# Kernel optimization log

Hardware: AMD Instinct MI355X
Metric: run time of the kernel (lower is better)

## Reference

```python
import jax, jax.numpy as jnp
import numpy as np

B, N, D = 16, 4096, 256
EPS = 1e-6


def setup_inputs() -> dict:
    key = jax.random.key(0)
    kq, kk, kv, kwq, kwk, kbq, kbk = jax.random.split(key, 7)
    s = 1.0 / np.sqrt(D)
    return {
        "Q": jax.random.normal(kq, (B, N, D), dtype=jnp.float32),
        "K": jax.random.normal(kk, (B, N, D), dtype=jnp.float32),
        "V": jax.random.normal(kv, (B, N, D), dtype=jnp.float32),
        "Wq": jax.random.normal(kwq, (D, D), dtype=jnp.float32) * s,
        "bq": jax.random.normal(kbq, (D,), dtype=jnp.float32) * 0.01,
        "Wk": jax.random.normal(kwk, (D, D), dtype=jnp.float32) * s,
        "bk": jax.random.normal(kbk, (D,), dtype=jnp.float32) * 0.01,
    }


def reference(Q, K, V, Wq, bq, Wk, bk):
    # phi feature maps: sigmoid(Linear(dim, dim)) as in Flow-Attention
    phi_q = jax.nn.sigmoid(jnp.einsum("bnd,de->bne", Q, Wq) + bq)  # [B,N,D]
    phi_k = jax.nn.sigmoid(jnp.einsum("bnd,de->bne", K, Wk) + bk)  # [B,N,D]
    # O: column-normalized phi_k (over sequence); I: row-normalized phi_q (over features)
    O = phi_k / (jnp.sum(phi_k, axis=1, keepdims=True) + EPS)  # [B,N,D]
    I = phi_q / (jnp.sum(phi_q, axis=2, keepdims=True) + EPS)  # [B,N,D]
    # competition over the sequence dim
    V_b = jax.nn.softmax(O * V, axis=1)  # [B,N,D]
    # linear attention: (phi_k^T @ V_b) is the small [B,D,D] state
    KV = jnp.einsum("bnd,bne->bde", phi_k, V_b)  # [B,D,D]
    A = jnp.einsum("bnd,bde->bne", I, KV)  # [B,N,D]
    # sigmoid allocation gate
    R = jax.nn.sigmoid(jnp.sum(phi_q, axis=2, keepdims=True)) * A
    return R
```

## Files before the change

kernel.cpp:

```cpp
#include <hip/hip_runtime.h>
#include <cstddef>

#define EPS_ 1e-6f

typedef unsigned short u16;
typedef __attribute__((ext_vector_type(8))) short short8;
typedef __attribute__((ext_vector_type(8))) unsigned short us8;
typedef __attribute__((ext_vector_type(4))) unsigned short us4;
typedef __attribute__((ext_vector_type(4))) float f32x4;

__device__ __forceinline__ float sigmoidf_(float x){ return 1.0f/(1.0f+__expf(-x)); }
__device__ __forceinline__ float sigmoidf_fast(float x){
  return __builtin_amdgcn_rcpf(1.0f+__expf(-x));
}
__device__ __forceinline__ u16 f2bf(float x){
  union { __bf16 b; u16 u; } c; c.b = (__bf16)x; return c.u;
}
__device__ __forceinline__ float bf2f(u16 u){
  union { unsigned i; float f; } c; c.i = ((unsigned)u) << 16; return c.f;
}
__device__ __forceinline__ us4 cvt4(float4 v){
  us4 h; h[0]=f2bf(v.x); h[1]=f2bf(v.y); h[2]=f2bf(v.z); h[3]=f2bf(v.w); return h;
}

__global__ __launch_bounds__(256) void prep_w(const float* __restrict__ Wq,
                                              const float* __restrict__ Wk,
                                              u16* __restrict__ WqT,
                                              u16* __restrict__ WkT){
  const int e = blockIdx.x & 255;
  const float* W = (blockIdx.x < 256) ? Wq : Wk;
  u16* WT = (blockIdx.x < 256) ? WqT : WkT;
  const int d = threadIdx.x;
  WT[e*256 + d] = f2bf(W[d*256 + e]);
}

__global__ __launch_bounds__(256, 3) void phi_both(
    const float* __restrict__ Q, const float* __restrict__ K,
    const u16* __restrict__ WqT, const u16* __restrict__ WkT,
    const float* __restrict__ bq, const float* __restrict__ bk,
    u16* __restrict__ phi_q, u16* __restrict__ phi_kT,
    float* __restrict__ rowsum, float* __restrict__ colsum)
{
  __shared__ union {
    u16 A[64][264];
    u16 S[64][264];
    u16 T2[128][136];
  } sh;

  const int t = threadIdx.x;
  const int l = t & 63;
  const int wf = t >> 6;
  const int i16 = l & 15, q = l >> 4;
  const int row0 = blockIdx.x * 64;
  const bool trans = (blockIdx.z != 0);

  const float* X    = trans ? K   : Q;
  const u16*  WT    = trans ? WkT : WqT;
  const float* bias = trans ? bk  : bq;

  {
    const int r0 = t >> 4;
    const int c0 = t & 15;
    #pragma unroll
    for (int half = 0; half < 2; half++) {
      float4 v[8];
      #pragma unroll
      for (int p = 0; p < 8; p++) {
        const int row = r0 + 16*(half*2 + (p >> 2));
        const int k4  = c0 + 16*(p & 3);
        v[p] = *(const float4*)&X[(size_t)(row0 + row)*256 + k4*4];
      }
      #pragma unroll
      for (int p = 0; p < 8; p++) {
        const int row = r0 + 16*(half*2 + (p >> 2));
        const int k4  = c0 + 16*(p & 3);
        *(us4*)&sh.A[row][k4*4] = cvt4(v[p]);
      }
    }
  }
  __syncthreads();

  f32x4 acc[4][4];
  #pragma unroll
  for (int i=0;i<4;i++)
    #pragma unroll
    for (int j=0;j<4;j++) acc[i][j] = (f32x4){0.f,0.f,0.f,0.f};

  const u16* wb = WT + (size_t)(wf*64 + i16)*256 + q*8;
  short8 Bfr[3][4];
  #pragma unroll
  for (int fi=0;fi<4;fi++) Bfr[0][fi] = *(const short8*)&wb[fi*4096];
  #pragma unroll
  for (int fi=0;fi<4;fi++) Bfr[1][fi] = *(const short8*)&wb[fi*4096 + 32];

  #pragma unroll
  for (int it = 0; it < 8; it++) {
    if (it < 6) {
      #pragma unroll
      for (int fi=0;fi<4;fi++)
        Bfr[(it+2)%3][fi] = *(const short8*)&wb[fi*4096 + (it+2)*32];
    }
    short8 af[4];
    #pragma unroll
    for (int mi=0;mi<4;mi++)
      af[mi] = *(const short8*)&sh.A[mi*16 + i16][it*32 + q*8];
    #pragma unroll
    for (int mi=0;mi<4;mi++)
      #pragma unroll
      for (int fi=0;fi<4;fi++)
        acc[mi][fi] = __builtin_amdgcn_mfma_f32_16x16x32_bf16(af[mi], Bfr[it%3][fi], acc[mi][fi], 0,0,0);
  }

  float bv[4];
  #pragma unroll
  for (int fi=0;fi<4;fi++) bv[fi] = bias[wf*64 + fi*16 + i16];

  __syncthreads();

  if (!trans) {
    #pragma unroll
    for (int mi=0;mi<4;mi++) {
      float rsub[4] = {0.f,0.f,0.f,0.f};
      #pragma unroll
      for (int fi=0;fi<4;fi++) {
        #pragma unroll
        for (int r=0;r<4;r++) {
          float ph = sigmoidf_fast(acc[mi][fi][r] + bv[fi]);
          rsub[r] += ph;
          sh.S[mi*16 + q*4 + r][wf*64 + fi*16 + i16] = f2bf(ph);
        }
      }
      #pragma unroll
      for (int r=0;r<4;r++) {
        float s = rsub[r];
        s += __shfl_xor(s,1); s += __shfl_xor(s,2); s += __shfl_xor(s,4); s += __shfl_xor(s,8);
        if (i16 == 0) atomicAdd(&rowsum[row0 + mi*16 + q*4 + r], s);
      }
    }
    __syncthreads();
    const size_t gbase = (size_t)row0 * 256;
    #pragma unroll
    for (int j=0;j<8;j++) {
      const int g = (j*256 + t) * 8;
      *(us8*)&phi_q[gbase + g] = *(const us8*)&sh.S[g >> 8][g & 255];
    }
  } else {
    const int b      = row0 >> 12;
    const int nchunk = (row0 & 4095) >> 6;
    #pragma unroll
    for (int h = 0; h < 2; h++) {
      if ((wf >> 1) == h) {
        #pragma unroll
        for (int fi=0;fi<4;fi++) {
          float cp = 0.f;
          #pragma unroll
          for (int mi=0;mi<4;mi++) {
            #pragma unroll
            for (int r=0;r<4;r++) {
              float ph = sigmoidf_fast(acc[mi][fi][r] + bv[fi]);
              cp += ph;
              sh.T2[(wf*64 + fi*16 + i16) & 127][mi*16 + q*4 + r] = f2bf(ph);
            }
          }
          cp += __shfl_xor(cp,16); cp += __shfl_xor(cp,32);
          if (l < 16) atomicAdd(&colsum[b*256 + wf*64 + fi*16 + l], cp);
        }
      }
      __syncthreads();
      const size_t gb = ((size_t)(b*64 + nchunk)*256 + h*128) * 64;
      #pragma unroll
      for (int j=0;j<4;j++) {
        const int g = (j*256 + t) * 8;
        *(us8*)&phi_kT[gb + g] = *(const us8*)&sh.T2[g >> 6][g & 63];
      }
      __syncthreads();
    }
  }
}

__global__ __launch_bounds__(256) void kv_kernel(const u16* __restrict__ phi_kT,
    const float* __restrict__ V, const float* __restrict__ colsum,
    u16* __restrict__ partsT, float* __restrict__ denom)
{
  __shared__ u16 phiT_lds[256][72];
  __shared__ u16 E_lds[64][72];

  const int t = threadIdx.x;
  const int l = t & 63;
  const int w = t >> 6;
  const int e0 = blockIdx.x * 64;
  const int nc = blockIdx.y;
  const int b  = blockIdx.z;
  const int i16 = l & 15, q = l >> 4;

  const int sd = t >> 3;
  const int sn = (t & 7) * 8;

  const size_t cbase = (size_t)(b*64 + nc*4) * 256 * 64;

  us8  rA[8];
  float rV[16];
  #pragma unroll
  for (int p=0;p<8;p++)
    rA[p] = *(const us8*)&phi_kT[cbase + (size_t)(sd + 32*p)*64 + sn];
  #pragma unroll
  for (int j=0;j<16;j++)
    rV[j] = V[(size_t)(b*4096 + nc*256 + w*16 + j)*256 + e0 + l];

  const float inv_cs = 1.0f / (colsum[b*256 + e0 + l] + EPS_);
  float dsum = 0.f;

  f32x4 acc[4][4];
  #pragma unroll
  for (int i=0;i<4;i++)
    #pragma unroll
    for (int j=0;j<4;j++) acc[i][j] = (f32x4){0.f,0.f,0.f,0.f};

  for (int c = 0; c < 4; c++) {
    #pragma unroll
    for (int p=0;p<8;p++) *(us8*)&phiT_lds[sd + 32*p][sn] = rA[p];
    __syncthreads();
    if (c < 3) {
      const size_t nb = cbase + (size_t)(c+1)*16384;
      #pragma unroll
      for (int p=0;p<8;p++)
        rA[p] = *(const us8*)&phi_kT[nb + (size_t)(sd + 32*p)*64 + sn];
    }
    us8 pv0 = *(const us8*)&phiT_lds[e0 + l][w*16];
    us8 pv1 = *(const us8*)&phiT_lds[e0 + l][w*16 + 8];
    us8 ev0, ev1;
    #pragma unroll
    for (int j=0;j<8;j++) {
      float ef = __expf(bf2f(pv0[j]) * inv_cs * rV[j]);
      dsum += ef; ev0[j] = f2bf(ef);
    }
    #pragma unroll
    for (int j=0;j<8;j++) {
      float ef = __expf(bf2f(pv1[j]) * inv_cs * rV[8+j]);
      dsum += ef; ev1[j] = f2bf(ef);
    }
    *(us8*)&E_lds[l][w*16]     = ev0;
    *(us8*)&E_lds[l][w*16 + 8] = ev1;
    if (c < 3) {
      #pragma unroll
      for (int j=0;j<16;j++)
        rV[j] = V[(size_t)(b*4096 + nc*256 + (c+1)*64 + w*16 + j)*256 + e0 + l];
    }
    __syncthreads();
    #pragma unroll
    for (int kk=0;kk<2;kk++){
      const int ko = kk*32 + q*8;
      short8 af[4], bfr[4];
      #pragma unroll
      for (int mi=0;mi<4;mi++) af[mi]  = *(const short8*)&phiT_lds[w*64 + mi*16 + i16][ko];
      #pragma unroll
      for (int ei=0;ei<4;ei++) bfr[ei] = *(const short8*)&E_lds[ei*16 + i16][ko];
      #pragma unroll
      for (int mi=0;mi<4;mi++)
        #pragma unroll
        for (int ei=0;ei<4;ei++)
          acc[mi][ei] = __builtin_amdgcn_mfma_f32_16x16x32_bf16(af[mi], bfr[ei], acc[mi][ei],0,0,0);
    }
    __syncthreads();
  }

  atomicAdd(&denom[b*256 + e0 + l], dsum);

  u16* slice = partsT + (size_t)(nc*16 + b) * 65536;
  #pragma unroll
  for (int mi=0;mi<4;mi++)
    #pragma unroll
    for (int ei=0;ei<4;ei++) {
      us4 o;
      #pragma unroll
      for (int r=0;r<4;r++) o[r] = f2bf(acc[mi][ei][r]);
      *(us4*)&slice[(size_t)(e0 + ei*16 + i16)*256 + w*64 + mi*16 + q*4] = o;
    }
}

__global__ __launch_bounds__(256) void kv_norm(const u16* __restrict__ partsT,
    const float* __restrict__ denom, u16* __restrict__ KV_nT)
{
  const int t = threadIdx.x;
  const int b = blockIdx.y;
  const size_t idx = (size_t)blockIdx.x * 1024 + t*4;
  const int e = (int)(idx >> 8);
  const float dn = denom[b*256 + e];
  float s0=0.f,s1=0.f,s2=0.f,s3=0.f;
  #pragma unroll 4
  for (int nc=0;nc<16;nc++){
    us4 v = *(const us4*)&partsT[(size_t)(nc*16 + b)*65536 + idx];
    s0+=bf2f(v[0]); s1+=bf2f(v[1]); s2+=bf2f(v[2]); s3+=bf2f(v[3]);
  }
  us4 o; o[0]=f2bf(s0/dn); o[1]=f2bf(s1/dn); o[2]=f2bf(s2/dn); o[3]=f2bf(s3/dn);
  *(us4*)&KV_nT[(size_t)b*65536 + idx] = o;
}

__global__ __launch_bounds__(256, 3) void out_gemm(const u16* __restrict__ phi_q,
    const u16* __restrict__ KV_nT, const float* __restrict__ rowsum,
    float* __restrict__ outp)
{
  __shared__ u16 A_lds[64][264];
  __shared__ float rs_lds[64];

  const int t = threadIdx.x;
  const int l = t & 63;
  const int we = t >> 6;
  const int i16 = l & 15, q = l >> 4;
  const int n0 = blockIdx.x * 64;
  const int b  = blockIdx.y;

  if (t < 64) rs_lds[t] = rowsum[b*4096 + n0 + t];

  {
    const size_t gbase = (size_t)(b*4096 + n0) * 256;
    us8 v[8];
    #pragma unroll
    for (int j=0;j<8;j++)
      v[j] = *(const us8*)&phi_q[gbase + (size_t)(j*256 + t)*8];
    #pragma unroll
    for (int j=0;j<8;j++) {
      const int g = (j*256 + t) * 8;
      *(us8*)&A_lds[g >> 8][g & 255] = v[j];
    }
  }
  __syncthreads();

  f32x4 acc[4][4];
  #pragma unroll
  for (int i=0;i<4;i++)
    #pragma unroll
    for (int j=0;j<4;j++) acc[i][j] = (f32x4){0.f,0.f,0.f,0.f};

  const u16* kb = KV_nT + (size_t)(b*256 + we*64 + i16)*256 + q*8;
  short8 Bfr[3][4];
  #pragma unroll
  for (int ei=0;ei<4;ei++) Bfr[0][ei] = *(const short8*)&kb[ei*4096];
  #pragma unroll
  for (int ei=0;ei<4;ei++) Bfr[1][ei] = *(const short8*)&kb[ei*4096 + 32];

  #pragma unroll
  for (int it=0; it<8; it++){
    if (it < 6) {
      #pragma unroll
      for (int ei=0;ei<4;ei++)
        Bfr[(it+2)%3][ei] = *(const short8*)&kb[ei*4096 + (it+2)*32];
    }
    short8 af[4];
    #pragma unroll
    for (int mi=0;mi<4;mi++)
      af[mi] = *(const short8*)&A_lds[mi*16 + i16][it*32 + q*8];
    #pragma unroll
    for (int mi=0;mi<4;mi++)
      #pragma unroll
      for (int ei=0;ei<4;ei++)
        acc[mi][ei] = __builtin_amdgcn_mfma_f32_16x16x32_bf16(af[mi], Bfr[it%3][ei], acc[mi][ei],0,0,0);
  }

  #pragma unroll
  for (int mi=0;mi<4;mi++){
    #pragma unroll
    for (int r=0;r<4;r++){
      const int nl = mi*16 + q*4 + r;
      const float rs = rs_lds[nl];
      const float gate = sigmoidf_(rs) / (rs + EPS_);
      #pragma unroll
      for (int ei=0;ei<4;ei++)
        outp[((size_t)(b*4096 + n0 + nl))*256 + we*64 + ei*16 + i16] = gate*acc[mi][ei][r];
    }
  }
}

extern "C" void kernel_launch(void* const* d_in, const int* in_sizes, int n_in,
                              void* d_out, int out_size, void* d_ws, size_t ws_size,
                              hipStream_t stream) {
  const float* Q  = (const float*)d_in[0];
  const float* K  = (const float*)d_in[1];
  const float* V  = (const float*)d_in[2];
  const float* Wq = (const float*)d_in[3];
  const float* bq = (const float*)d_in[4];
  const float* Wk = (const float*)d_in[5];
  const float* bk = (const float*)d_in[6];
  float* out = (float*)d_out;

  u16* phi_q  = (u16*)d_ws;
  u16* phi_kT = phi_q + 16777216;
  u16* WqT    = phi_kT + 16777216;
  u16* WkT    = WqT + 65536;
  float* colsum = (float*)(WkT + 65536);
  float* denom  = colsum + 4096;
  float* rowsum = denom + 4096;
  u16* partsT = (u16*)(rowsum + 65536);
  u16* KV_nT  = partsT + 16777216;

  hipMemsetAsync(colsum, 0, (4096 + 4096 + 65536) * sizeof(float), stream);

  prep_w<<<dim3(512), 256, 0, stream>>>(Wq, Wk, WqT, WkT);
  phi_both<<<dim3(1024, 1, 2), 256, 0, stream>>>(Q, K, WqT, WkT, bq, bk,
                                                 phi_q, phi_kT, rowsum, colsum);
  kv_kernel<<<dim3(4, 16, 16), 256, 0, stream>>>(phi_kT, V, colsum, partsT, denom);
  kv_norm<<<dim3(64, 16), 256, 0, stream>>>(partsT, denom, KV_nT);
  out_gemm<<<dim3(64, 16), 256, 0, stream>>>(phi_q, KV_nT, rowsum, out);
}
```

Before: 300.4 us.

## Store weight and KV matrices in MFMA fragment-packed layout for coalesced B loads

```diff
diff --git a/kernel.cpp b/kernel.cpp
--- a/kernel.cpp
+++ b/kernel.cpp
@@ -27,11 +27,24 @@
                                               const float* __restrict__ Wk,
                                               u16* __restrict__ WqT,
                                               u16* __restrict__ WkT){
-  const int e = blockIdx.x & 255;
-  const float* W = (blockIdx.x < 256) ? Wq : Wk;
-  u16* WT = (blockIdx.x < 256) ? WqT : WkT;
-  const int d = threadIdx.x;
-  WT[e*256 + d] = f2bf(W[d*256 + e]);
+  const int m  = blockIdx.x >> 4;
+  const int eb = blockIdx.x & 15;
+  const float* W = m ? Wk : Wq;
+  u16* WTf = m ? WkT : WqT;
+  const int t = threadIdx.x;
+  #pragma unroll
+  for (int rep = 0; rep < 2; rep++) {
+    const int lin  = rep*256 + t;
+    const int it   = lin >> 6;
+    const int lane = lin & 63;
+    const int q    = lane >> 4;
+    const int i16  = lane & 15;
+    us8 o;
+    #pragma unroll
+    for (int j = 0; j < 8; j++)
+      o[j] = f2bf(W[(it*32 + q*8 + j)*256 + eb*16 + i16]);
+    *(us8*)&WTf[(size_t)((eb*8 + it)*512 + lane*8)] = o;
+  }
 }
 
 __global__ __launch_bounds__(256, 3) void phi_both(
@@ -86,19 +99,19 @@
     #pragma unroll
     for (int j=0;j<4;j++) acc[i][j] = (f32x4){0.f,0.f,0.f,0.f};
 
-  const u16* wb = WT + (size_t)(wf*64 + i16)*256 + q*8;
+  const u16* wbf = WT + (size_t)wf*16384 + (size_t)l*8;
   short8 Bfr[3][4];
   #pragma unroll
-  for (int fi=0;fi<4;fi++) Bfr[0][fi] = *(const short8*)&wb[fi*4096];
-  #pragma unroll
-  for (int fi=0;fi<4;fi++) Bfr[1][fi] = *(const short8*)&wb[fi*4096 + 32];
+  for (int fi=0;fi<4;fi++) Bfr[0][fi] = *(const short8*)&wbf[fi*4096];
+  #pragma unroll
+  for (int fi=0;fi<4;fi++) Bfr[1][fi] = *(const short8*)&wbf[fi*4096 + 512];
 
   #pragma unroll
   for (int it = 0; it < 8; it++) {
     if (it < 6) {
       #pragma unroll
       for (int fi=0;fi<4;fi++)
-        Bfr[(it+2)%3][fi] = *(const short8*)&wb[fi*4096 + (it+2)*32];
+        Bfr[(it+2)%3][fi] = *(const short8*)&wbf[fi*4096 + (it+2)*512];
     }
     short8 af[4];
     #pragma unroll
@@ -266,7 +279,7 @@
 
   atomicAdd(&denom[b*256 + e0 + l], dsum);
 
-  u16* slice = partsT + (size_t)(nc*16 + b) * 65536;
+  u16* slice = partsT + (size_t)(nc*16 + b) * 65536 + (size_t)blockIdx.x * 16384;
   #pragma unroll
   for (int mi=0;mi<4;mi++)
     #pragma unroll
@@ -274,7 +287,7 @@
       us4 o;
       #pragma unroll
       for (int r=0;r<4;r++) o[r] = f2bf(acc[mi][ei][r]);
-      *(us4*)&slice[(size_t)(e0 + ei*16 + i16)*256 + w*64 + mi*16 + q*4] = o;
+      *(us4*)&slice[(size_t)(((w*16 + mi*4 + ei)*64 + l)*4)] = o;
     }
 }
 
@@ -283,17 +296,32 @@
 {
   const int t = threadIdx.x;
   const int b = blockIdx.y;
-  const size_t idx = (size_t)blockIdx.x * 1024 + t*4;
-  const int e = (int)(idx >> 8);
+  const int s4 = blockIdx.x*256 + t;
+  const int e0b = s4 >> 12;
+  const int rem = s4 & 4095;
+  const int comb = rem >> 6;
+  const int l = rem & 63;
+  const int w  = comb >> 4;
+  const int mi = (comb >> 2) & 3;
+  const int ei = comb & 3;
+  const int e  = e0b*64 + ei*16 + (l & 15);
+  const int d0 = w*64 + mi*16 + (l >> 4)*4;
+
   const float dn = denom[b*256 + e];
   float s0=0.f,s1=0.f,s2=0.f,s3=0.f;
   #pragma unroll 4
   for (int nc=0;nc<16;nc++){
-    us4 v = *(const us4*)&partsT[(size_t)(nc*16 + b)*65536 + idx];
+    us4 v = *(const us4*)&partsT[(size_t)(nc*16 + b)*65536 + (size_t)s4*4];
     s0+=bf2f(v[0]); s1+=bf2f(v[1]); s2+=bf2f(v[2]); s3+=bf2f(v[3]);
   }
   us4 o; o[0]=f2bf(s0/dn); o[1]=f2bf(s1/dn); o[2]=f2bf(s2/dn); o[3]=f2bf(s3/dn);
-  *(us4*)&KV_nT[(size_t)b*65536 + idx] = o;
+
+  const int eb  = e >> 4;
+  const int i16 = e & 15;
+  const int it  = d0 >> 5;
+  const int qo  = (d0 >> 3) & 3;
+  const int j0  = d0 & 4;
+  *(us4*)&KV_nT[(size_t)b*65536 + (size_t)((eb*8 + it)*512 + (qo*16 + i16)*8 + j0)] = o;
 }
 
 __global__ __launch_bounds__(256, 3) void out_gemm(const u16* __restrict__ phi_q,
@@ -332,19 +360,19 @@
     #pragma unroll
     for (int j=0;j<4;j++) acc[i][j] = (f32x4){0.f,0.f,0.f,0.f};
 
-  const u16* kb = KV_nT + (size_t)(b*256 + we*64 + i16)*256 + q*8;
+  const u16* kbf = KV_nT + (size_t)b*65536 + (size_t)we*16384 + (size_t)l*8;
   short8 Bfr[3][4];
   #pragma unroll
-  for (int ei=0;ei<4;ei++) Bfr[0][ei] = *(const short8*)&kb[ei*4096];
-  #pragma unroll
-  for (int ei=0;ei<4;ei++) Bfr[1][ei] = *(const short8*)&kb[ei*4096 + 32];
+  for (int ei=0;ei<4;ei++) Bfr[0][ei] = *(const short8*)&kbf[ei*4096];
+  #pragma unroll
+  for (int ei=0;ei<4;ei++) Bfr[1][ei] = *(const short8*)&kbf[ei*4096 + 512];
 
   #pragma unroll
   for (int it=0; it<8; it++){
     if (it < 6) {
       #pragma unroll
       for (int ei=0;ei<4;ei++)
-        Bfr[(it+2)%3][ei] = *(const short8*)&kb[ei*4096 + (it+2)*32];
+        Bfr[(it+2)%3][ei] = *(const short8*)&kbf[ei*4096 + (it+2)*512];
     }
     short8 af[4];
     #pragma unroll
@@ -395,7 +423,7 @@
 
   hipMemsetAsync(colsum, 0, (4096 + 4096 + 65536) * sizeof(float), stream);
 
-  prep_w<<<dim3(512), 256, 0, stream>>>(Wq, Wk, WqT, WkT);
+  prep_w<<<dim3(32), 256, 0, stream>>>(Wq, Wk, WqT, WkT);
   phi_both<<<dim3(1024, 1, 2), 256, 0, stream>>>(Q, K, WqT, WkT, bq, bk,
                                                  phi_q, phi_kT, rowsum, colsum);
   kv_kernel<<<dim3(4, 16, 16), 256, 0, stream>>>(phi_kT, V, colsum, partsT, denom);
```

After: 287.0 us. 4.5% less time.
